# Kernel tuning notes

Hardware: AMD Instinct MI355X
Metric: run time of the kernel (lower is better)

## Reference

```python
import jax, jax.numpy as jnp
import numpy as np

N = 50000
E = 800000
NFEAT, NHID, NCLASS = 128, 64, 16


def _spmm(row, col, w, x):
    # out[i] = sum_{e: row[e]==i} w[e] * x[col[e]]  -- sparse adj @ x
    return jax.ops.segment_sum(x[col] * w[:, None], row, num_segments=N)


def _gcn_layer(x, row, col, w, W, b):
    return _spmm(row, col, w, x @ W) + b


def setup_inputs() -> dict:
    key = jax.random.key(0)
    ks = jax.random.split(key, 16)
    glorot = lambda k, fi, fo: jax.random.uniform(k, (fi, fo), jnp.float32, -1.0, 1.0) / jnp.sqrt(fi)
    inp = {
        "x": jax.random.normal(ks[0], (N, NFEAT), jnp.float32),
        "edge_row": jax.random.randint(ks[1], (E,), 0, N, jnp.int32),
        "edge_col": jax.random.randint(ks[2], (E,), 0, N, jnp.int32),
        "edge_weight": jax.random.uniform(ks[3], (E,), jnp.float32),
        "W1": glorot(ks[4], NFEAT, NHID), "b1": jnp.zeros((NHID,), jnp.float32),
        "W2": glorot(ks[5], NHID, NHID), "b2": jnp.zeros((NHID,), jnp.float32),
        "W3": glorot(ks[6], NHID, NHID), "b3": jnp.zeros((NHID,), jnp.float32),
        "W4": glorot(ks[7], NHID, NHID), "b4": jnp.zeros((NHID,), jnp.float32),
        "W5": glorot(ks[8], NHID, NCLASS), "b5": jnp.zeros((NCLASS,), jnp.float32),
    }
    return inp


def reference(x, edge_row, edge_col, edge_weight, W1, b1, W2, b2, W3, b3, W4, b4, W5, b5):
    # Inference mode: dropout is identity.
    e1 = _gcn_layer(x, edge_row, edge_col, edge_weight, W1, b1)
    h = jax.nn.relu(e1)
    e2 = _gcn_layer(h, edge_row, edge_col, edge_weight, W2, b2)
    h = jax.nn.relu(e2)
    e3 = _gcn_layer(h, edge_row, edge_col, edge_weight, W3, b3)
    h = jax.nn.relu(e3)
    e4 = _gcn_layer(h, edge_row, edge_col, edge_weight, W4, b4)
    h = jax.nn.relu(e4)
    e5 = _gcn_layer(h, edge_row, edge_col, edge_weight, W5, b5)
    return (jax.nn.log_softmax(e5, axis=1), e1, e2, e3, e4, e5)
```

## Files before the change

kernel.cpp:

```cpp
#include <hip/hip_runtime.h>
#include <math.h>

#define NN 50000
#define NE 800000
#define NFEAT 128
#define NHID 64
#define NCLASS 16
#define NB_SCAN ((NN + 255) / 256)
#define GB ((NN + 63) / 64)

__device__ inline unsigned short f2bf(float f) {
    unsigned u = __builtin_bit_cast(unsigned, f);
    u += 0x7fffu + ((u >> 16) & 1u);
    return (unsigned short)(u >> 16);
}
__device__ inline float bf2f(unsigned short h) {
    return __builtin_bit_cast(float, (unsigned)h << 16);
}
__device__ inline float pk_w(unsigned v) { return bf2f((unsigned short)(v >> 16)); }
__device__ inline int pk_c(unsigned v) { return (int)(v & 0xffffu); }


__global__ __launch_bounds__(256) void hist_kernel(const int* __restrict__ erow,
                                                   int* __restrict__ deg, int E) {
    int e = blockIdx.x * 256 + threadIdx.x;
    if (e < E) atomicAdd(&deg[erow[e]], 1);
}

__global__ __launch_bounds__(256) void scan_sum_kernel(const int* __restrict__ deg,
                                                       int* __restrict__ blocksum, int n) {
    __shared__ int s[256];
    const int t = threadIdx.x;
    int i = blockIdx.x * 256 + t;
    s[t] = (i < n) ? deg[i] : 0;
    __syncthreads();
#pragma unroll
    for (int off = 128; off > 0; off >>= 1) {
        if (t < off) s[t] += s[t + off];
        __syncthreads();
    }
    if (t == 0) blocksum[blockIdx.x] = s[0];
}

__global__ __launch_bounds__(256) void scan_final_kernel(const int* __restrict__ deg,
                                                         const int* __restrict__ blocksum,
                                                         int* __restrict__ row_ptr,
                                                         int* __restrict__ cursor, int n) {
    __shared__ int bs[256];
    __shared__ int s[256];
    const int t = threadIdx.x;
    bs[t] = (t < NB_SCAN) ? blocksum[t] : 0;
    __syncthreads();
    for (int off = 1; off < 256; off <<= 1) {
        int u = (t >= off) ? bs[t - off] : 0;
        __syncthreads();
        bs[t] += u;
        __syncthreads();
    }
    const int blockpre = (blockIdx.x == 0) ? 0 : bs[blockIdx.x - 1];

    int i = blockIdx.x * 256 + t;
    int d = (i < n) ? deg[i] : 0;
    s[t] = d;
    __syncthreads();
    for (int off = 1; off < 256; off <<= 1) {
        int u = (t >= off) ? s[t - off] : 0;
        __syncthreads();
        s[t] += u;
        __syncthreads();
    }
    int excl = blockpre + s[t] - d;
    if (i < n) {
        row_ptr[i] = excl;
        cursor[i] = excl;
        if (i == n - 1) row_ptr[n] = excl + d;
    }
}

__global__ __launch_bounds__(256) void scatter_atomic_kernel(const int* __restrict__ erow,
                                                             const int* __restrict__ ecol,
                                                             const float* __restrict__ ew,
                                                             int* __restrict__ cursor,
                                                             unsigned* __restrict__ pk, int E) {
    int e = blockIdx.x * 256 + threadIdx.x;
    if (e < E) {
        int r = erow[e];
        int pos = atomicAdd(&cursor[r], 1);
        pk[pos] = ((unsigned)f2bf(ew[e]) << 16) | (unsigned)ecol[e];
    }
}

template <int K, bool RELU_IN>
__global__ __launch_bounds__(256) void gemm64_kernel(const float* __restrict__ in,
                                                     const float* __restrict__ Wg,
                                                     unsigned short* __restrict__ outb, int M) {
    constexpr int KC = 64;
    __shared__ float xs[KC][68];
    __shared__ float Ws[KC][64];
    const int t = threadIdx.x;
    const int tx = t % 16;
    const int ty = t / 16;
    const int r0 = blockIdx.x * 64;

    float acc[4][4];
#pragma unroll
    for (int i = 0; i < 4; i++)
#pragma unroll
        for (int j = 0; j < 4; j++) acc[i][j] = 0.f;

    for (int k0 = 0; k0 < K; k0 += KC) {
        for (int i = t * 4; i < KC * 64; i += 1024) {
            *(float4*)&Ws[i / 64][i % 64] = *(const float4*)&Wg[(size_t)k0 * 64 + i];
        }
        {
            const int r = t / 4;
            const int q = t % 4;
            const int gr = r0 + r;
#pragma unroll
            for (int i = 0; i < 4; i++) {
                int k = q * 16 + i * 4;
                float4 v;
                if (gr < M)
                    v = *(const float4*)&in[(size_t)gr * K + k0 + k];
                else
                    v = make_float4(0.f, 0.f, 0.f, 0.f);
                if (RELU_IN) {
                    v.x = fmaxf(v.x, 0.f);
                    v.y = fmaxf(v.y, 0.f);
                    v.z = fmaxf(v.z, 0.f);
                    v.w = fmaxf(v.w, 0.f);
                }
                xs[k + 0][r] = v.x;
                xs[k + 1][r] = v.y;
                xs[k + 2][r] = v.z;
                xs[k + 3][r] = v.w;
            }
        }
        __syncthreads();
#pragma unroll 8
        for (int k = 0; k < KC; k++) {
            float4 xv = *(const float4*)&xs[k][ty * 4];
            float4 wv = *(const float4*)&Ws[k][tx * 4];
            acc[0][0] += xv.x * wv.x; acc[0][1] += xv.x * wv.y;
            acc[0][2] += xv.x * wv.z; acc[0][3] += xv.x * wv.w;
            acc[1][0] += xv.y * wv.x; acc[1][1] += xv.y * wv.y;
            acc[1][2] += xv.y * wv.z; acc[1][3] += xv.y * wv.w;
            acc[2][0] += xv.z * wv.x; acc[2][1] += xv.z * wv.y;
            acc[2][2] += xv.z * wv.z; acc[2][3] += xv.z * wv.w;
            acc[3][0] += xv.w * wv.x; acc[3][1] += xv.w * wv.y;
            acc[3][2] += xv.w * wv.z; acc[3][3] += xv.w * wv.w;
        }
        __syncthreads();
    }
#pragma unroll
    for (int i = 0; i < 4; i++) {
        int r = r0 + ty * 4 + i;
        if (r < M) {
            ushort4 u;
            u.x = f2bf(acc[i][0]);
            u.y = f2bf(acc[i][1]);
            u.z = f2bf(acc[i][2]);
            u.w = f2bf(acc[i][3]);
            *(ushort4*)&outb[(size_t)r * 64 + tx * 4] = u;
        }
    }
}

template <int NOUT>
__global__ __launch_bounds__(512) void spmm64_fused_kernel(
    const unsigned short* __restrict__ gb,
    const int* __restrict__ row_ptr,
    const unsigned* __restrict__ pk,
    const float* __restrict__ bias,
    const float* __restrict__ Wn,
    float* __restrict__ e_out,
    unsigned short* __restrict__ nxt,
    int M) {
    __shared__ float Wlt[NOUT][65];
    __shared__ float xs[8][64];
    const int t = threadIdx.x;

    for (int idx = t; idx < 64 * NOUT; idx += 512) {
        int k = idx / NOUT, j = idx % NOUT;
        Wlt[j][k] = Wn[idx];
    }

    const int wv = __builtin_amdgcn_readfirstlane(t >> 6);
    const int lane = t & 63;
    int r = blockIdx.x * 8 + wv;
    if (r >= M) r = M - 1;

    float a = 0.f;
    int e = row_ptr[r];
    const int end = row_ptr[r + 1];
    for (; e + 8 <= end; e += 8) {
        unsigned q0 = pk[e + 0], q1 = pk[e + 1], q2 = pk[e + 2], q3 = pk[e + 3];
        unsigned q4 = pk[e + 4], q5 = pk[e + 5], q6 = pk[e + 6], q7 = pk[e + 7];
        a += pk_w(q0) * bf2f(gb[(size_t)pk_c(q0) * 64 + lane]);
        a += pk_w(q1) * bf2f(gb[(size_t)pk_c(q1) * 64 + lane]);
        a += pk_w(q2) * bf2f(gb[(size_t)pk_c(q2) * 64 + lane]);
        a += pk_w(q3) * bf2f(gb[(size_t)pk_c(q3) * 64 + lane]);
        a += pk_w(q4) * bf2f(gb[(size_t)pk_c(q4) * 64 + lane]);
        a += pk_w(q5) * bf2f(gb[(size_t)pk_c(q5) * 64 + lane]);
        a += pk_w(q6) * bf2f(gb[(size_t)pk_c(q6) * 64 + lane]);
        a += pk_w(q7) * bf2f(gb[(size_t)pk_c(q7) * 64 + lane]);
    }
    for (; e < end; ++e) {
        unsigned q = pk[e];
        a += pk_w(q) * bf2f(gb[(size_t)pk_c(q) * 64 + lane]);
    }
    float v = a + bias[lane];
    e_out[(size_t)r * 64 + lane] = v;
    xs[wv][lane] = fmaxf(v, 0.f);
    __syncthreads();

    if (NOUT == 64) {
        const int rr = t >> 6;
        const int j = t & 63;
        float acc = 0.f;
#pragma unroll 16
        for (int k = 0; k < 64; k++) acc += xs[rr][k] * Wlt[j][k];
        int gr = blockIdx.x * 8 + rr;
        if (gr < M) nxt[(size_t)gr * 64 + j] = f2bf(acc);
    } else {
        if (t < 8 * NOUT) {
            const int rr = t / NOUT;
            const int j = t % NOUT;
            float acc = 0.f;
#pragma unroll 16
            for (int k = 0; k < 64; k++) acc += xs[rr][k] * Wlt[j][k];
            int gr = blockIdx.x * 8 + rr;
            if (gr < M) nxt[(size_t)gr * NOUT + j] = f2bf(acc);
        }
    }
}

__global__ __launch_bounds__(256) void spmm16_lsm_kernel(const unsigned short* __restrict__ tmpc,
                                                         const int* __restrict__ row_ptr,
                                                         const unsigned* __restrict__ pk,
                                                         const float* __restrict__ bias,
                                                         float* __restrict__ e5,
                                                         float* __restrict__ out0, int M) {
    const int t = threadIdx.x;
    const int wv = __builtin_amdgcn_readfirstlane(t >> 6);
    const int lane = t & 63;
    const int f = lane & 15;
    const int s = lane >> 4;
    const int r = blockIdx.x * 4 + wv;
    if (r >= M) return;

    int e = row_ptr[r];
    const int end = row_ptr[r + 1];
    float acc = 0.f;
    for (; e + 8 <= end; e += 8) {
        unsigned qa = pk[e + s];
        unsigned qb = pk[e + 4 + s];
        acc += pk_w(qa) * bf2f(tmpc[(size_t)pk_c(qa) * 16 + f]);
        acc += pk_w(qb) * bf2f(tmpc[(size_t)pk_c(qb) * 16 + f]);
    }
    if (e + 4 <= end) {
        unsigned q = pk[e + s];
        acc += pk_w(q) * bf2f(tmpc[(size_t)pk_c(q) * 16 + f]);
        e += 4;
    }
    if (s < end - e) {
        unsigned q = pk[e + s];
        acc += pk_w(q) * bf2f(tmpc[(size_t)pk_c(q) * 16 + f]);
    }
    acc += __shfl_xor(acc, 16);
    acc += __shfl_xor(acc, 32);
    float v = acc + bias[f];

    float m = v;
#pragma unroll
    for (int off = 1; off < 16; off <<= 1) m = fmaxf(m, __shfl_xor(m, off, 16));
    float sum = expf(v - m);
#pragma unroll
    for (int off = 1; off < 16; off <<= 1) sum += __shfl_xor(sum, off, 16);
    float ls = logf(sum);
    if (lane < 16) {
        e5[(size_t)r * 16 + f] = v;
        out0[(size_t)r * 16 + f] = v - m - ls;
    }
}


extern "C" void kernel_launch(void* const* d_in, const int* in_sizes, int n_in,
                              void* d_out, int out_size, void* d_ws, size_t ws_size,
                              hipStream_t stream) {
    const float* x = (const float*)d_in[0];
    const int* erow = (const int*)d_in[1];
    const int* ecol = (const int*)d_in[2];
    const float* ew = (const float*)d_in[3];
    const float* W1 = (const float*)d_in[4];
    const float* b1 = (const float*)d_in[5];
    const float* W2 = (const float*)d_in[6];
    const float* b2 = (const float*)d_in[7];
    const float* W3 = (const float*)d_in[8];
    const float* b3 = (const float*)d_in[9];
    const float* W4 = (const float*)d_in[10];
    const float* b4 = (const float*)d_in[11];
    const float* W5 = (const float*)d_in[12];
    const float* b5 = (const float*)d_in[13];

    float* out0 = (float*)d_out;
    float* e1 = out0 + (size_t)NN * NCLASS;
    float* e2 = e1 + (size_t)NN * NHID;
    float* e3 = e2 + (size_t)NN * NHID;
    float* e4 = e3 + (size_t)NN * NHID;
    float* e5 = e4 + (size_t)NN * NHID;

    char* ws = (char*)d_ws;
    unsigned short* tmpA = (unsigned short*)ws; ws += (size_t)NN * NHID * 2;
    unsigned short* tmpB = (unsigned short*)ws; ws += (size_t)NN * NHID * 2;
    unsigned short* tmpc = (unsigned short*)ws; ws += ((size_t)NN * NCLASS * 2 + 255) / 256 * 256;
    int* deg = (int*)ws;      ws += ((size_t)NN * 4 + 255) / 256 * 256;
    int* row_ptr = (int*)ws;  ws += ((size_t)(NN + 1) * 4 + 255) / 256 * 256;
    int* cursor = (int*)ws;   ws += ((size_t)NN * 4 + 255) / 256 * 256;
    int* blocksum = (int*)ws; ws += ((size_t)NB_SCAN * 4 + 255) / 256 * 256;
    unsigned* pk = (unsigned*)ws; ws += (size_t)NE * 4;

    hipMemsetAsync(deg, 0, (size_t)NN * 4, stream);
    hist_kernel<<<(NE + 255) / 256, 256, 0, stream>>>(erow, deg, NE);
    scan_sum_kernel<<<NB_SCAN, 256, 0, stream>>>(deg, blocksum, NN);
    scan_final_kernel<<<NB_SCAN, 256, 0, stream>>>(deg, blocksum, row_ptr, cursor, NN);
    scatter_atomic_kernel<<<(NE + 255) / 256, 256, 0, stream>>>(erow, ecol, ew, cursor, pk, NE);

    gemm64_kernel<NFEAT, false><<<GB, 256, 0, stream>>>(x, W1, tmpA, NN);

    const int FG = NN / 8;
    spmm64_fused_kernel<64><<<FG, 512, 0, stream>>>(tmpA, row_ptr, pk, b1, W2, e1, tmpB, NN);
    spmm64_fused_kernel<64><<<FG, 512, 0, stream>>>(tmpB, row_ptr, pk, b2, W3, e2, tmpA, NN);
    spmm64_fused_kernel<64><<<FG, 512, 0, stream>>>(tmpA, row_ptr, pk, b3, W4, e3, tmpB, NN);
    spmm64_fused_kernel<16><<<FG, 512, 0, stream>>>(tmpB, row_ptr, pk, b4, W5, e4, tmpc, NN);

    spmm16_lsm_kernel<<<(NN + 3) / 4, 256, 0, stream>>>(tmpc, row_ptr, pk, b5, e5, out0, NN);
}
```

Before: 381.6 us.

## Record edge slot in histogram pass and scatter CSR per-XCD row partition

The histogram kernel now captures each edge's slot within its row from the degree atomic and stores a packed (row, slot, weight, col) record. This removes the second atomic pass over a cursor array. A new scatter kernel has each XCD, identified through the XCC_ID hardware register, handle writes only for its own eighth of the rows. Chunks are pulled from a per-group work queue so that pk and row_ptr writes stay local to one XCD's L2. The cost is an extra 6.4MB intermediate buffer and each edge record being read by up to eight groups, with correctness relying on 16-bit row and slot packing (rows below 65536).

```diff
diff --git a/kernel.cpp b/kernel.cpp
--- a/kernel.cpp
+++ b/kernel.cpp
@@ -8,6 +8,8 @@
 #define NCLASS 16
 #define NB_SCAN ((NN + 255) / 256)
 #define GB ((NN + 63) / 64)
+#define SC_CHUNKS 128
+#define ROWS_G8 ((NN + 7) / 8)
 
 __device__ inline unsigned short f2bf(float f) {
     unsigned u = __builtin_bit_cast(unsigned, f);
@@ -21,10 +23,20 @@
 __device__ inline int pk_c(unsigned v) { return (int)(v & 0xffffu); }
 
 
-__global__ __launch_bounds__(256) void hist_kernel(const int* __restrict__ erow,
-                                                   int* __restrict__ deg, int E) {
+__global__ __launch_bounds__(256) void hist_pack_kernel(const int* __restrict__ erow,
+                                                        const int* __restrict__ ecol,
+                                                        const float* __restrict__ ew,
+                                                        int* __restrict__ deg,
+                                                        uint2* __restrict__ rr8, int E) {
     int e = blockIdx.x * 256 + threadIdx.x;
-    if (e < E) atomicAdd(&deg[erow[e]], 1);
+    if (e < E) {
+        int r = erow[e];
+        int k = atomicAdd(&deg[r], 1);
+        uint2 v;
+        v.x = ((unsigned)r << 16) | (unsigned)k;
+        v.y = ((unsigned)f2bf(ew[e]) << 16) | (unsigned)ecol[e];
+        rr8[e] = v;
+    }
 }
 
 __global__ __launch_bounds__(256) void scan_sum_kernel(const int* __restrict__ deg,
@@ -44,8 +56,7 @@
 
 __global__ __launch_bounds__(256) void scan_final_kernel(const int* __restrict__ deg,
                                                          const int* __restrict__ blocksum,
-                                                         int* __restrict__ row_ptr,
-                                                         int* __restrict__ cursor, int n) {
+                                                         int* __restrict__ row_ptr, int n) {
     __shared__ int bs[256];
     __shared__ int s[256];
     const int t = threadIdx.x;
@@ -72,21 +83,40 @@
     int excl = blockpre + s[t] - d;
     if (i < n) {
         row_ptr[i] = excl;
-        cursor[i] = excl;
         if (i == n - 1) row_ptr[n] = excl + d;
     }
 }
 
-__global__ __launch_bounds__(256) void scatter_atomic_kernel(const int* __restrict__ erow,
-                                                             const int* __restrict__ ecol,
-                                                             const float* __restrict__ ew,
-                                                             int* __restrict__ cursor,
-                                                             unsigned* __restrict__ pk, int E) {
-    int e = blockIdx.x * 256 + threadIdx.x;
-    if (e < E) {
-        int r = erow[e];
-        int pos = atomicAdd(&cursor[r], 1);
-        pk[pos] = ((unsigned)f2bf(ew[e]) << 16) | (unsigned)ecol[e];
+__global__ __launch_bounds__(256) void scatter8_kernel(const uint2* __restrict__ rr8,
+                                                       const int* __restrict__ row_ptr,
+                                                       int* __restrict__ qcur,
+                                                       unsigned* __restrict__ pk, int E) {
+    __shared__ int s_chunk;
+    const int t = threadIdx.x;
+    int myg;
+    asm volatile("s_getreg_b32 %0, hwreg(HW_REG_XCC_ID, 0, 32)" : "=s"(myg));
+    myg &= 7;
+    const int CH = (E + SC_CHUNKS - 1) / SC_CHUNKS;
+    for (int gg = 0; gg < 8; gg++) {
+        const int g = (myg + gg) & 7;
+        const int rlo = g * ROWS_G8;
+        const int rhi = (rlo + ROWS_G8 < NN) ? rlo + ROWS_G8 : NN;
+        for (;;) {
+            if (t == 0) s_chunk = atomicAdd(&qcur[g], 1);
+            __syncthreads();
+            const int chunk = s_chunk;
+            __syncthreads();
+            if (chunk >= SC_CHUNKS) break;
+            const int lo = chunk * CH;
+            const int hi = (lo + CH < E) ? lo + CH : E;
+            for (int e = lo + t; e < hi; e += 256) {
+                uint2 v = rr8[e];
+                int r = (int)(v.x >> 16);
+                if (r >= rlo && r < rhi) {
+                    pk[row_ptr[r] + (int)(v.x & 0xffffu)] = v.y;
+                }
+            }
+        }
     }
 }
 
@@ -314,17 +344,18 @@
     unsigned short* tmpA = (unsigned short*)ws; ws += (size_t)NN * NHID * 2;
     unsigned short* tmpB = (unsigned short*)ws; ws += (size_t)NN * NHID * 2;
     unsigned short* tmpc = (unsigned short*)ws; ws += ((size_t)NN * NCLASS * 2 + 255) / 256 * 256;
+    int* qcur = (int*)ws;     ws += 256;
     int* deg = (int*)ws;      ws += ((size_t)NN * 4 + 255) / 256 * 256;
     int* row_ptr = (int*)ws;  ws += ((size_t)(NN + 1) * 4 + 255) / 256 * 256;
-    int* cursor = (int*)ws;   ws += ((size_t)NN * 4 + 255) / 256 * 256;
     int* blocksum = (int*)ws; ws += ((size_t)NB_SCAN * 4 + 255) / 256 * 256;
+    uint2* rr8 = (uint2*)ws;  ws += (size_t)NE * 8;
     unsigned* pk = (unsigned*)ws; ws += (size_t)NE * 4;
 
-    hipMemsetAsync(deg, 0, (size_t)NN * 4, stream);
-    hist_kernel<<<(NE + 255) / 256, 256, 0, stream>>>(erow, deg, NE);
+    hipMemsetAsync(qcur, 0, 256 + (size_t)NN * 4, stream);
+    hist_pack_kernel<<<(NE + 255) / 256, 256, 0, stream>>>(erow, ecol, ew, deg, rr8, NE);
     scan_sum_kernel<<<NB_SCAN, 256, 0, stream>>>(deg, blocksum, NN);
-    scan_final_kernel<<<NB_SCAN, 256, 0, stream>>>(deg, blocksum, row_ptr, cursor, NN);
-    scatter_atomic_kernel<<<(NE + 255) / 256, 256, 0, stream>>>(erow, ecol, ew, cursor, pk, NE);
+    scan_final_kernel<<<NB_SCAN, 256, 0, stream>>>(deg, blocksum, row_ptr, NN);
+    scatter8_kernel<<<8 * SC_CHUNKS, 256, 0, stream>>>(rr8, row_ptr, qcur, pk, NE);
 
     gemm64_kernel<NFEAT, false><<<GB, 256, 0, stream>>>(x, W1, tmpA, NN);
 
```

Result: slower. 461.6 us (+21.0%).
